# Kernel tuning notes

Measured on AMD Instinct MI355X. Metric: run time of the kernel, lower is better.

Reference implementation:

```python
import jax, jax.numpy as jnp
import numpy as np

POSTFIX = jnp.array([[1.0, 0.0, 1.0, 0.0],
                     [0.0, 1.0, 0.0, 1.0],
                     [-0.5, 0.0, 0.5, 0.0],
                     [0.0, -0.5, 0.0, 0.5]], dtype=jnp.float32)


def roi_pool(feat, rois_scaled, out_h=16, out_w=8):
    # feat: [B,C,H,W]; rois_scaled: [B,4] float (x1,y1,x2,y2 in pixel units).
    # Faithful to torch: rois.long() truncation, slice y1:y2+1 / x1:x2+1 (end clipped
    # to H/W), then F.adaptive_max_pool2d with PyTorch bin boundaries
    # start=floor(i*h/out), end=ceil((i+1)*h/out).
    H, W = feat.shape[2], feat.shape[3]
    r = rois_scaled.astype(jnp.int32)  # values are >= 0 after clamp, trunc == floor

    def one(f, ri):  # f: [C,H,W], ri: [4] int32
        x1, y1 = ri[0], ri[1]
        x2 = jnp.minimum(ri[2], W - 1)  # slice end clipping
        y2 = jnp.minimum(ri[3], H - 1)
        h = y2 - y1 + 1
        w = x2 - x1 + 1
        # column bins
        j = jnp.arange(out_w)
        cs = x1 + (j * w) // out_w
        ce = x1 + ((j + 1) * w + out_w - 1) // out_w  # ceil
        cols = jnp.arange(W)
        cmask = (cols[None, :] >= cs[:, None]) & (cols[None, :] < ce[:, None])  # [out_w,W]
        t = jnp.max(jnp.where(cmask[:, None, None, :], f[None], -jnp.inf), axis=3)  # [out_w,C,H]
        # row bins
        i = jnp.arange(out_h)
        rs = y1 + (i * h) // out_h
        re = y1 + ((i + 1) * h + out_h - 1) // out_h
        rows = jnp.arange(H)
        rmask = (rows[None, :] >= rs[:, None]) & (rows[None, :] < re[:, None])  # [out_h,H]
        out = jnp.max(jnp.where(rmask[:, None, None, :], t[None], -jnp.inf), axis=3)  # [out_h,out_w,C]
        return jnp.transpose(out, (2, 0, 1))  # [C,out_h,out_w]

    return jax.vmap(one)(feat, r)


def setup_inputs() -> dict:
    key = jax.random.key(0)
    ks = jax.random.split(key, 12)
    B = 16
    return {
        "box_xywh": jax.random.uniform(ks[0], (B, 4), dtype=jnp.float32),
        "x2": jax.random.normal(ks[1], (B, 64, 128, 128), dtype=jnp.float32),
        "x4": jax.random.normal(ks[2], (B, 160, 64, 64), dtype=jnp.float32),
        "x6": jax.random.normal(ks[3], (B, 192, 32, 32), dtype=jnp.float32),
        "Wh": jax.random.normal(ks[4], (7, 53248, 128), dtype=jnp.float32) * 0.01,
        "bh": jax.random.normal(ks[5], (7, 128), dtype=jnp.float32) * 0.01,
        "Wp": jax.random.normal(ks[6], (128, 38), dtype=jnp.float32) * 0.05,
        "bp": jax.random.normal(ks[7], (38,), dtype=jnp.float32) * 0.05,
        "Wa": jax.random.normal(ks[8], (128, 25), dtype=jnp.float32) * 0.05,
        "ba": jax.random.normal(ks[9], (25,), dtype=jnp.float32) * 0.05,
        "Wd": jax.random.normal(ks[10], (5, 128, 35), dtype=jnp.float32) * 0.05,
        "bd": jax.random.normal(ks[11], (5, 35), dtype=jnp.float32) * 0.05,
    }


def reference(box_xywh, x2, x4, x6, Wh, bh, Wp, bp, Wa, ba, Wd, bd):
    B = box_xywh.shape[0]
    box_xyxy = jnp.clip(box_xywh @ POSTFIX, 0.0, 1.0)  # [B,4]
    # Faithful to original: x coords scaled by size(2)=H, y coords by size(3)=W.
    def scale(feat):
        H, W = feat.shape[2], feat.shape[3]
        return box_xyxy * jnp.array([H, W, H, W], dtype=box_xyxy.dtype)
    p1 = roi_pool(x2, scale(x2))   # [B,64,16,8]
    p2 = roi_pool(x4, scale(x4))   # [B,160,16,8]
    p3 = roi_pool(x6, scale(x6))   # [B,192,16,8]
    rois = jnp.concatenate([p1, p2, p3], axis=1).reshape(B, -1)  # [B,53248]
    hid = jnp.einsum('bf,kfh->kbh', rois, Wh) + bh[:, None, :]   # [7,B,128]
    o1 = hid[0] @ Wp + bp                                        # [B,38]
    o2 = hid[1] @ Wa + ba                                        # [B,25]
    od = jnp.einsum('kbh,kho->bko', hid[2:], Wd) + bd[None]      # [B,5,35]
    return jnp.concatenate([box_xywh, o1, o2, od.reshape(B, -1)], axis=1)  # [B,242]
```

## Files before the change

### kernel.cpp

```cpp
#include <hip/hip_runtime.h>
#include <math.h>


#define B 16
#define F_TOT 53248
#define FC 512
#define NCHUNK (F_TOT / FC)

__device__ __forceinline__ float clamp01(float v) {
    return fminf(fmaxf(v, 0.0f), 1.0f);
}

__global__ void roi_kernel(const float* __restrict__ feat,
                           const float* __restrict__ box,
                           float* __restrict__ rois,
                           int C, int S, int fbase) {
    int t = blockIdx.x * blockDim.x + threadIdx.x;
    int total = B * C * 128;
    if (t >= total) return;
    int j = t & 7;
    int i = (t >> 3) & 15;
    int c = (t >> 7) % C;
    int b = t / (C << 7);

    const float* bx = box + b * 4;
    float x = bx[0], y = bx[1], wd = bx[2], ht = bx[3];
    float Sf = (float)S;
    int x1 = (int)(clamp01(x - 0.5f * wd) * Sf);
    int y1 = (int)(clamp01(y - 0.5f * ht) * Sf);
    int x2 = (int)(clamp01(x + 0.5f * wd) * Sf);
    int y2 = (int)(clamp01(y + 0.5f * ht) * Sf);
    x2 = min(x2, S - 1);
    y2 = min(y2, S - 1);
    int h = y2 - y1 + 1;
    int w = x2 - x1 + 1;

    int rs = y1 + (i * h) / 16;
    int re = y1 + ((i + 1) * h + 15) / 16;
    int cs = x1 + (j * w) / 8;
    int ce = x1 + ((j + 1) * w + 7) / 8;

    const float* fp = feat + ((size_t)(b * C + c)) * S * S;
    float m = -INFINITY;
    for (int r = rs; r < re; ++r) {
        const float* row = fp + r * S;
        for (int cc = cs; cc < ce; ++cc) m = fmaxf(m, row[cc]);
    }
    int f = fbase + (c * 16 + i) * 8 + j;
    rois[(size_t)b * F_TOT + f] = m;
}

__global__ __launch_bounds__(256) void matmul_part(const float* __restrict__ rois,
                                                   const float* __restrict__ Wh,
                                                   float* __restrict__ partial) {
    __shared__ float rs_[FC * 16];
    const int cid = blockIdx.x;
    const int k = blockIdx.y;
    const int f0 = cid * FC;
    const int tid = threadIdx.x;

    for (int idx = tid; idx < FC * 16; idx += 256) {
        int b = idx & 15;
        int fl = idx >> 4;
        rs_[idx] = rois[(size_t)b * F_TOT + f0 + fl];
    }
    __syncthreads();

    const int h = tid & 127;
    const int fo = tid >> 7;
    const float* wp = Wh + ((size_t)k * F_TOT + f0 + fo) * 128 + h;

    float acc[16];
#pragma unroll
    for (int b = 0; b < 16; ++b) acc[b] = 0.0f;

#pragma unroll 4
    for (int fl = fo; fl < FC; fl += 2) {
        float w = *wp;
        wp += 256;
        const float4* rp = (const float4*)(rs_ + (fl << 4));
        float4 r0 = rp[0], r1 = rp[1], r2 = rp[2], r3 = rp[3];
        acc[0]  += r0.x * w; acc[1]  += r0.y * w; acc[2]  += r0.z * w; acc[3]  += r0.w * w;
        acc[4]  += r1.x * w; acc[5]  += r1.y * w; acc[6]  += r1.z * w; acc[7]  += r1.w * w;
        acc[8]  += r2.x * w; acc[9]  += r2.y * w; acc[10] += r2.z * w; acc[11] += r2.w * w;
        acc[12] += r3.x * w; acc[13] += r3.y * w; acc[14] += r3.z * w; acc[15] += r3.w * w;
    }

    __syncthreads();
    if (fo) {
#pragma unroll
        for (int b = 0; b < 16; ++b) rs_[b * 128 + h] = acc[b];
    }
    __syncthreads();
    if (!fo) {
        float* op = partial + ((size_t)(k * NCHUNK + cid)) * (B * 128);
#pragma unroll
        for (int b = 0; b < 16; ++b) op[b * 128 + h] = acc[b] + rs_[b * 128 + h];
    }
}

__global__ void reduce_kernel(const float* __restrict__ partial,
                              const float* __restrict__ bh,
                              float* __restrict__ hid) {
    int t = blockIdx.x * blockDim.x + threadIdx.x;
    int k = t / (B * 128);
    int r = t % (B * 128);
    int h = r & 127;
    float s = bh[k * 128 + h];
    const float* pp = partial + (size_t)k * NCHUNK * (B * 128) + r;
    for (int cid = 0; cid < NCHUNK; ++cid) s += pp[(size_t)cid * (B * 128)];
    hid[t] = s;
}

__global__ void head_kernel(const float* __restrict__ hid,
                            const float* __restrict__ box,
                            const float* __restrict__ Wp, const float* __restrict__ bp,
                            const float* __restrict__ Wa, const float* __restrict__ ba,
                            const float* __restrict__ Wd, const float* __restrict__ bd,
                            float* __restrict__ out) {
    __shared__ float hs[7 * 128];
    const int b = blockIdx.x;
    const int j = threadIdx.x;
    for (int idx = j; idx < 7 * 128; idx += 256) {
        int k = idx >> 7;
        int h = idx & 127;
        hs[idx] = hid[k * (B * 128) + b * 128 + h];
    }
    __syncthreads();
    if (j >= 242) return;
    float v;
    if (j < 4) {
        v = box[b * 4 + j];
    } else if (j < 42) {
        int o = j - 4;
        v = bp[o];
        for (int h = 0; h < 128; ++h) v += hs[h] * Wp[h * 38 + o];
    } else if (j < 67) {
        int o = j - 42;
        v = ba[o];
        for (int h = 0; h < 128; ++h) v += hs[128 + h] * Wa[h * 25 + o];
    } else {
        int t = j - 67;
        int kk = t / 35;
        int o = t % 35;
        v = bd[kk * 35 + o];
        for (int h = 0; h < 128; ++h) v += hs[(2 + kk) * 128 + h] * Wd[(kk * 128 + h) * 35 + o];
    }
    out[b * 242 + j] = v;
}

extern "C" void kernel_launch(void* const* d_in, const int* in_sizes, int n_in,
                              void* d_out, int out_size, void* d_ws, size_t ws_size,
                              hipStream_t stream) {
    const float* box = (const float*)d_in[0];
    const float* x2  = (const float*)d_in[1];
    const float* x4  = (const float*)d_in[2];
    const float* x6  = (const float*)d_in[3];
    const float* Wh  = (const float*)d_in[4];
    const float* bh  = (const float*)d_in[5];
    const float* Wp  = (const float*)d_in[6];
    const float* bp  = (const float*)d_in[7];
    const float* Wa  = (const float*)d_in[8];
    const float* ba  = (const float*)d_in[9];
    const float* Wd  = (const float*)d_in[10];
    const float* bd  = (const float*)d_in[11];
    float* out = (float*)d_out;

    float* ws = (float*)d_ws;
    float* rois    = ws;
    float* partial = ws + (size_t)B * F_TOT;
    float* hid     = partial + (size_t)7 * NCHUNK * B * 128;

    roi_kernel<<<(B * 64  * 128) / 256, 256, 0, stream>>>(x2, box, rois, 64, 128, 0);
    roi_kernel<<<(B * 160 * 128) / 256, 256, 0, stream>>>(x4, box, rois, 160, 64, 8192);
    roi_kernel<<<(B * 192 * 128) / 256, 256, 0, stream>>>(x6, box, rois, 192, 32, 28672);

    matmul_part<<<dim3(NCHUNK, 7), 256, 0, stream>>>(rois, Wh, partial);
    reduce_kernel<<<(7 * B * 128) / 256, 256, 0, stream>>>(partial, bh, hid);

    head_kernel<<<B, 256, 0, stream>>>(hid, box, Wp, bp, Wa, ba, Wd, bd, out);
}
```

Baseline: 402.5 us.

## Register-tile Wh matmul over two columns and fuse ROI and tail kernels

The matmul now has each thread compute two adjacent hidden columns, loading them as a float2 and reusing each shared-memory ROI float4 for two outputs. Four f-slices are reduced through shared memory. This halves the LDS traffic per FMA but uses more accumulator registers. The three ROI pooling launches are merged into one block-dispatched kernel, and the chunk reduction is folded into the head kernel, removing launches and the hid round-trip. The fused tail runs only 16 blocks, so the reduction parallelism drops.

```diff
diff --git a/kernel.cpp b/kernel.cpp
--- a/kernel.cpp
+++ b/kernel.cpp
@@ -11,13 +11,18 @@
     return fminf(fmaxf(v, 0.0f), 1.0f);
 }
 
-__global__ void roi_kernel(const float* __restrict__ feat,
-                           const float* __restrict__ box,
-                           float* __restrict__ rois,
-                           int C, int S, int fbase) {
-    int t = blockIdx.x * blockDim.x + threadIdx.x;
-    int total = B * C * 128;
-    if (t >= total) return;
+__global__ __launch_bounds__(256) void roi_all(const float* __restrict__ x2,
+                                               const float* __restrict__ x4,
+                                               const float* __restrict__ x6,
+                                               const float* __restrict__ box,
+                                               float* __restrict__ rois) {
+    const int blk = blockIdx.x;
+    const float* feat;
+    int C, S, fbase, t;
+    if (blk < 512)       { feat = x2; C = 64;  S = 128; fbase = 0;     t = blk * 256 + threadIdx.x; }
+    else if (blk < 1792) { feat = x4; C = 160; S = 64;  fbase = 8192;  t = (blk - 512) * 256 + threadIdx.x; }
+    else                 { feat = x6; C = 192; S = 32;  fbase = 28672; t = (blk - 1792) * 256 + threadIdx.x; }
+
     int j = t & 7;
     int i = (t >> 3) & 15;
     int c = (t >> 7) % C;
@@ -28,12 +33,12 @@
     float Sf = (float)S;
     int x1 = (int)(clamp01(x - 0.5f * wd) * Sf);
     int y1 = (int)(clamp01(y - 0.5f * ht) * Sf);
-    int x2 = (int)(clamp01(x + 0.5f * wd) * Sf);
-    int y2 = (int)(clamp01(y + 0.5f * ht) * Sf);
-    x2 = min(x2, S - 1);
-    y2 = min(y2, S - 1);
-    int h = y2 - y1 + 1;
-    int w = x2 - x1 + 1;
+    int x2i = (int)(clamp01(x + 0.5f * wd) * Sf);
+    int y2i = (int)(clamp01(y + 0.5f * ht) * Sf);
+    x2i = min(x2i, S - 1);
+    y2i = min(y2i, S - 1);
+    int h = y2i - y1 + 1;
+    int w = x2i - x1 + 1;
 
     int rs = y1 + (i * h) / 16;
     int re = y1 + ((i + 1) * h + 15) / 16;
@@ -66,67 +71,65 @@
     }
     __syncthreads();
 
-    const int h = tid & 127;
-    const int fo = tid >> 7;
-    const float* wp = Wh + ((size_t)k * F_TOT + f0 + fo) * 128 + h;
+    const int fo = tid >> 6;
+    const int h0 = (tid & 63) * 2;
+    const float* wp = Wh + ((size_t)k * F_TOT + f0 + fo) * 128 + h0;
 
-    float acc[16];
+    float a0[16], a1[16];
 #pragma unroll
-    for (int b = 0; b < 16; ++b) acc[b] = 0.0f;
+    for (int b = 0; b < 16; ++b) { a0[b] = 0.0f; a1[b] = 0.0f; }
 
 #pragma unroll 4
-    for (int fl = fo; fl < FC; fl += 2) {
-        float w = *wp;
-        wp += 256;
+    for (int fl = fo; fl < FC; fl += 4) {
+        float2 w = *(const float2*)wp;
+        wp += 512;
         const float4* rp = (const float4*)(rs_ + (fl << 4));
-        float4 r0 = rp[0], r1 = rp[1], r2 = rp[2], r3 = rp[3];
-        acc[0]  += r0.x * w; acc[1]  += r0.y * w; acc[2]  += r0.z * w; acc[3]  += r0.w * w;
-        acc[4]  += r1.x * w; acc[5]  += r1.y * w; acc[6]  += r1.z * w; acc[7]  += r1.w * w;
-        acc[8]  += r2.x * w; acc[9]  += r2.y * w; acc[10] += r2.z * w; acc[11] += r2.w * w;
-        acc[12] += r3.x * w; acc[13] += r3.y * w; acc[14] += r3.z * w; acc[15] += r3.w * w;
+#pragma unroll
+        for (int q = 0; q < 4; ++q) {
+            float4 rv = rp[q];
+            a0[q * 4 + 0] += rv.x * w.x;  a1[q * 4 + 0] += rv.x * w.y;
+            a0[q * 4 + 1] += rv.y * w.x;  a1[q * 4 + 1] += rv.y * w.y;
+            a0[q * 4 + 2] += rv.z * w.x;  a1[q * 4 + 2] += rv.z * w.y;
+            a0[q * 4 + 3] += rv.w * w.x;  a1[q * 4 + 3] += rv.w * w.y;
+        }
     }
 
     __syncthreads();
-    if (fo) {
 #pragma unroll
-        for (int b = 0; b < 16; ++b) rs_[b * 128 + h] = acc[b];
+    for (int b = 0; b < 16; ++b) {
+        *(float2*)(rs_ + fo * 2048 + b * 128 + h0) = make_float2(a0[b], a1[b]);
     }
     __syncthreads();
-    if (!fo) {
-        float* op = partial + ((size_t)(k * NCHUNK + cid)) * (B * 128);
-#pragma unroll
-        for (int b = 0; b < 16; ++b) op[b * 128 + h] = acc[b] + rs_[b * 128 + h];
+
+    float* op = partial + ((size_t)(k * NCHUNK + cid)) * (B * 128);
+    for (int idx = tid; idx < 2048; idx += 256) {
+        op[idx] = rs_[idx] + rs_[idx + 2048] + rs_[idx + 4096] + rs_[idx + 6144];
     }
 }
 
-__global__ void reduce_kernel(const float* __restrict__ partial,
-                              const float* __restrict__ bh,
-                              float* __restrict__ hid) {
-    int t = blockIdx.x * blockDim.x + threadIdx.x;
-    int k = t / (B * 128);
-    int r = t % (B * 128);
-    int h = r & 127;
-    float s = bh[k * 128 + h];
-    const float* pp = partial + (size_t)k * NCHUNK * (B * 128) + r;
-    for (int cid = 0; cid < NCHUNK; ++cid) s += pp[(size_t)cid * (B * 128)];
-    hid[t] = s;
-}
-
-__global__ void head_kernel(const float* __restrict__ hid,
-                            const float* __restrict__ box,
-                            const float* __restrict__ Wp, const float* __restrict__ bp,
-                            const float* __restrict__ Wa, const float* __restrict__ ba,
-                            const float* __restrict__ Wd, const float* __restrict__ bd,
-                            float* __restrict__ out) {
+__global__ __launch_bounds__(256) void tail_kernel(const float* __restrict__ partial,
+                                                   const float* __restrict__ bh,
+                                                   const float* __restrict__ box,
+                                                   const float* __restrict__ Wp, const float* __restrict__ bp,
+                                                   const float* __restrict__ Wa, const float* __restrict__ ba,
+                                                   const float* __restrict__ Wd, const float* __restrict__ bd,
+                                                   float* __restrict__ out) {
     __shared__ float hs[7 * 128];
     const int b = blockIdx.x;
-    const int j = threadIdx.x;
-    for (int idx = j; idx < 7 * 128; idx += 256) {
+    const int tid = threadIdx.x;
+
+    for (int idx = tid; idx < 7 * 128; idx += 256) {
         int k = idx >> 7;
         int h = idx & 127;
-        hs[idx] = hid[k * (B * 128) + b * 128 + h];
+        const float* pp = partial + (size_t)k * NCHUNK * (B * 128) + b * 128 + h;
+        float s = bh[idx];
+#pragma unroll 8
+        for (int cid = 0; cid < NCHUNK; ++cid) s += pp[(size_t)cid * (B * 128)];
+        hs[idx] = s;
     }
     __syncthreads();
+
+    const int j = tid;
     if (j >= 242) return;
     float v;
     if (j < 4) {
@@ -169,14 +172,8 @@
     float* ws = (float*)d_ws;
     float* rois    = ws;
     float* partial = ws + (size_t)B * F_TOT;
-    float* hid     = partial + (size_t)7 * NCHUNK * B * 128;
 
-    roi_kernel<<<(B * 64  * 128) / 256, 256, 0, stream>>>(x2, box, rois, 64, 128, 0);
-    roi_kernel<<<(B * 160 * 128) / 256, 256, 0, stream>>>(x4, box, rois, 160, 64, 8192);
-    roi_kernel<<<(B * 192 * 128) / 256, 256, 0, stream>>>(x6, box, rois, 192, 32, 28672);
-
+    roi_all<<<3328, 256, 0, stream>>>(x2, x4, x6, box, rois);
     matmul_part<<<dim3(NCHUNK, 7), 256, 0, stream>>>(rois, Wh, partial);
-    reduce_kernel<<<(7 * B * 128) / 256, 256, 0, stream>>>(partial, bh, hid);
-
-    head_kernel<<<B, 256, 0, stream>>>(hid, box, Wp, bp, Wa, ba, Wd, bd, out);
+    tail_kernel<<<B, 256, 0, stream>>>(partial, bh, box, Wp, bp, Wa, ba, Wd, bd, out);
 }
```

New measurement: 401.5 us. No clear change (-0.2%).
